# Optimization experiments

Measured on AMD Instinct MI355X. Metric: run time of the kernel, lower is better.

## Reference

```python
import jax, jax.numpy as jnp
import numpy as np

MAX_DUR = 4      # durations sampled in [0, 4], so padded output len = Tmax * MAX_DUR
PAD_VALUE = 0.0  # LengthRegulator pad_value


def setup_inputs() -> dict:
    key = jax.random.key(0)
    k1, k2 = jax.random.split(key)
    B, T, D = 16, 1024, 384
    xs = jax.random.normal(k1, (B, T, D), dtype=jnp.float32)
    ds = jax.random.randint(k2, (B, T), 0, MAX_DUR + 1, dtype=jnp.int32)
    return {"xs": xs, "ds": ds}


def reference(xs, ds):
    """Duration-based repeat-interleave + pad (FastSpeech length regulator).

    Equivalent math to: [repeat_interleave(x, d, dim=0) for x, d in zip(xs, ds)]
    followed by pad_list(..., pad_value), except the padded length is the static
    capacity T*MAX_DUR instead of the data-dependent batch max (extra columns
    are pure pad_value). For output frame t of sample b, the source token is
    the i with cumsum(ds)[b, i-1] <= t < cumsum(ds)[b, i].
    """
    B, T, D = xs.shape
    out_len = T * MAX_DUR  # static output capacity

    cs = jnp.cumsum(ds, axis=1)                      # (B, T) cumulative durations
    t = jnp.arange(out_len, dtype=cs.dtype)          # (out_len,)
    # source index per output frame: count of cumsums <= t
    idx = jax.vmap(lambda c: jnp.searchsorted(c, t, side="right"))(cs)  # (B, out_len)
    valid = t[None, :] < cs[:, -1:]                  # (B, out_len) within total length
    idx = jnp.minimum(idx, T - 1)

    gathered = jnp.take_along_axis(xs, idx[:, :, None], axis=1)  # (B, out_len, D)
    return jnp.where(valid[:, :, None], gathered, jnp.asarray(PAD_VALUE, xs.dtype))
```

## Files before the change

kernel.cpp:

```cpp
#include <hip/hip_runtime.h>
#include <hip/hip_bf16.h>

#define B_SZ 16
#define T_SZ 1024
#define D_SZ 384
#define MAX_DUR 4
#define OUT_LEN (T_SZ * MAX_DUR)
#define C4 (D_SZ / 4)
#define PER_SAMPLE_F4 (OUT_LEN * C4)
#define BLOCKS_PER_SAMPLE 96
#define ITERS 16

__global__ __launch_bounds__(256) void lenreg_fused(const float4* __restrict__ xs4,
                                                    const int* __restrict__ ds,
                                                    float4* __restrict__ out4) {
    __shared__ int sums[256];
    __shared__ int map[OUT_LEN];
    __shared__ int s_total;

    const int tid = threadIdx.x;
    const int b   = blockIdx.x / BLOCKS_PER_SAMPLE;
    const int blk = blockIdx.x - b * BLOCKS_PER_SAMPLE;

    int4 v = ((const int4*)(ds + b * T_SZ))[tid];
    const int s0 = v.x;
    const int s1 = s0 + v.y;
    const int s2 = s1 + v.z;
    const int s3 = s2 + v.w;

    sums[tid] = s3;
    __syncthreads();

    int val = s3;
    for (int off = 1; off < 256; off <<= 1) {
        int other = (tid >= off) ? sums[tid - off] : 0;
        __syncthreads();
        val += other;
        sums[tid] = val;
        __syncthreads();
    }
    const int excl = val - s3;
    if (tid == 255) s_total = val;

    const int srcBase = (b * T_SZ + 4 * tid) * C4;
    {
        int st = excl, en = excl + s0;
        for (int t = st; t < en; ++t) map[t] = srcBase;
        st = en; en = excl + s1;
        for (int t = st; t < en; ++t) map[t] = srcBase + C4;
        st = en; en = excl + s2;
        for (int t = st; t < en; ++t) map[t] = srcBase + 2 * C4;
        st = en; en = excl + s3;
        for (int t = st; t < en; ++t) map[t] = srcBase + 3 * C4;
    }
    __syncthreads();

    const int total = s_total;
    for (int t = total + tid; t < OUT_LEN; t += 256) map[t] = -1;
    __syncthreads();

    const int base = blk * (ITERS * 256);
    float4* outp = out4 + (size_t)b * PER_SAMPLE_F4;
    #pragma unroll
    for (int k = 0; k < ITERS; ++k) {
        const int g   = base + k * 256 + tid;
        const int f   = g / C4;
        const int col = g - f * C4;
        const int s   = map[f];
        float4 o = make_float4(0.0f, 0.0f, 0.0f, 0.0f);
        if (s >= 0) o = xs4[s + col];
        outp[g] = o;
    }
}

extern "C" void kernel_launch(void* const* d_in, const int* in_sizes, int n_in,
                              void* d_out, int out_size, void* d_ws, size_t ws_size,
                              hipStream_t stream) {
    const float4* xs4 = (const float4*)d_in[0];
    const int*    ds  = (const int*)d_in[1];
    float4*       out4 = (float4*)d_out;

    lenreg_fused<<<B_SZ * BLOCKS_PER_SAMPLE, 256, 0, stream>>>(xs4, ds, out4);
}
```

Measured before the change: 127.6 us.

## Use wave-shuffle scan, per-block frame window map, and nontemporal stores

Replaces the shared-memory Hillis-Steele scan with a wavefront shuffle scan plus a four-wave offset combine, cutting barriers. Each block now builds only the 32-frame slice of the frame-to-source map it needs instead of the full 4096-entry map, which shrinks LDS use and allows higher occupancy (launch bounds 256,8). Output writes use nontemporal stores to avoid polluting cache with the large streaming output, and the grid grows to 128 blocks per sample.

```diff
diff --git a/kernel.cpp b/kernel.cpp
--- a/kernel.cpp
+++ b/kernel.cpp
@@ -1,5 +1,4 @@
 #include <hip/hip_runtime.h>
-#include <hip/hip_bf16.h>
 
 #define B_SZ 16
 #define T_SZ 1024
@@ -8,77 +7,83 @@
 #define OUT_LEN (T_SZ * MAX_DUR)
 #define C4 (D_SZ / 4)
 #define PER_SAMPLE_F4 (OUT_LEN * C4)
-#define BLOCKS_PER_SAMPLE 96
-#define ITERS 16
+#define BLOCKS_PER_SAMPLE 128
+#define FRAMES_PER_BLOCK 32
+#define F4_PER_BLOCK (FRAMES_PER_BLOCK * C4)
+#define ITERS (F4_PER_BLOCK / 256)
 
-__global__ __launch_bounds__(256) void lenreg_fused(const float4* __restrict__ xs4,
+typedef float f32x4 __attribute__((ext_vector_type(4)));
+
+__global__ __launch_bounds__(256, 8) void lenreg_v2(const f32x4* __restrict__ xs4,
                                                     const int* __restrict__ ds,
-                                                    float4* __restrict__ out4) {
-    __shared__ int sums[256];
-    __shared__ int map[OUT_LEN];
-    __shared__ int s_total;
+                                                    f32x4* __restrict__ out4) {
+    __shared__ int map_s[FRAMES_PER_BLOCK];
+    __shared__ int wsum[4];
 
-    const int tid = threadIdx.x;
-    const int b   = blockIdx.x / BLOCKS_PER_SAMPLE;
-    const int blk = blockIdx.x - b * BLOCKS_PER_SAMPLE;
+    const int tid  = threadIdx.x;
+    const int lane = tid & 63;
+    const int w    = tid >> 6;
+    const int b    = blockIdx.x >> 7;
+    const int blk  = blockIdx.x & (BLOCKS_PER_SAMPLE - 1);
+    const int w0   = blk * FRAMES_PER_BLOCK;
 
-    int4 v = ((const int4*)(ds + b * T_SZ))[tid];
+    const int4 v = ((const int4*)(ds + b * T_SZ))[tid];
     const int s0 = v.x;
     const int s1 = s0 + v.y;
     const int s2 = s1 + v.z;
     const int s3 = s2 + v.w;
 
-    sums[tid] = s3;
+    int incl = s3;
+    #pragma unroll
+    for (int off = 1; off < 64; off <<= 1) {
+        const int n = __shfl_up(incl, off, 64);
+        if (lane >= off) incl += n;
+    }
+    if (lane == 63) wsum[w] = incl;
+    if (tid < FRAMES_PER_BLOCK) map_s[tid] = -1;
     __syncthreads();
 
-    int val = s3;
-    for (int off = 1; off < 256; off <<= 1) {
-        int other = (tid >= off) ? sums[tid - off] : 0;
-        __syncthreads();
-        val += other;
-        sums[tid] = val;
-        __syncthreads();
-    }
-    const int excl = val - s3;
-    if (tid == 255) s_total = val;
+    int woff = 0;
+    #pragma unroll
+    for (int i = 0; i < 4; ++i) woff += (i < w) ? wsum[i] : 0;
+    const int excl = woff + (incl - s3);
 
-    const int srcBase = (b * T_SZ + 4 * tid) * C4;
     {
-        int st = excl, en = excl + s0;
-        for (int t = st; t < en; ++t) map[t] = srcBase;
+        const int srcBase = 4 * tid * C4;
+        const int w1 = w0 + FRAMES_PER_BLOCK;
+        int st = excl;
+        int en = excl + s0;
+        for (int t = (st > w0 ? st : w0); t < (en < w1 ? en : w1); ++t) map_s[t - w0] = srcBase;
         st = en; en = excl + s1;
-        for (int t = st; t < en; ++t) map[t] = srcBase + C4;
+        for (int t = (st > w0 ? st : w0); t < (en < w1 ? en : w1); ++t) map_s[t - w0] = srcBase + C4;
         st = en; en = excl + s2;
-        for (int t = st; t < en; ++t) map[t] = srcBase + 2 * C4;
+        for (int t = (st > w0 ? st : w0); t < (en < w1 ? en : w1); ++t) map_s[t - w0] = srcBase + 2 * C4;
         st = en; en = excl + s3;
-        for (int t = st; t < en; ++t) map[t] = srcBase + 3 * C4;
+        for (int t = (st > w0 ? st : w0); t < (en < w1 ? en : w1); ++t) map_s[t - w0] = srcBase + 3 * C4;
     }
     __syncthreads();
 
-    const int total = s_total;
-    for (int t = total + tid; t < OUT_LEN; t += 256) map[t] = -1;
-    __syncthreads();
+    const f32x4* __restrict__ xsb  = xs4 + (size_t)b * (T_SZ * C4);
+    f32x4* __restrict__ outp = out4 + (size_t)b * PER_SAMPLE_F4 + (size_t)w0 * C4;
 
-    const int base = blk * (ITERS * 256);
-    float4* outp = out4 + (size_t)b * PER_SAMPLE_F4;
-    #pragma unroll
+    #pragma unroll 4
     for (int k = 0; k < ITERS; ++k) {
-        const int g   = base + k * 256 + tid;
-        const int f   = g / C4;
-        const int col = g - f * C4;
-        const int s   = map[f];
-        float4 o = make_float4(0.0f, 0.0f, 0.0f, 0.0f);
-        if (s >= 0) o = xs4[s + col];
-        outp[g] = o;
+        const unsigned l   = (unsigned)(k * 256 + tid);
+        const unsigned f   = l / 96u;
+        const unsigned col = l - f * 96u;
+        const int s = map_s[f];
+        f32x4 o = {0.0f, 0.0f, 0.0f, 0.0f};
+        if (s >= 0) o = xsb[s + col];
+        __builtin_nontemporal_store(o, outp + l);
     }
 }
 
 extern "C" void kernel_launch(void* const* d_in, const int* in_sizes, int n_in,
                               void* d_out, int out_size, void* d_ws, size_t ws_size,
                               hipStream_t stream) {
-    const float4* xs4 = (const float4*)d_in[0];
-    const int*    ds  = (const int*)d_in[1];
-    float4*       out4 = (float4*)d_out;
+    const f32x4* xs4 = (const f32x4*)d_in[0];
+    const int*   ds  = (const int*)d_in[1];
+    f32x4*       out4 = (f32x4*)d_out;
 
-    lenreg_fused<<<B_SZ * BLOCKS_PER_SAMPLE, 256, 0, stream>>>(xs4, ds, out4);
+    lenreg_v2<<<B_SZ * BLOCKS_PER_SAMPLE, 256, 0, stream>>>(xs4, ds, out4);
 }
```

Measured after the change: 137.2 us. 1.08x slower.
